# Kernel tuning notes

Measured on AMD Instinct MI355X. Metric: run time of the kernel, lower is better.

## Reference

```python
import jax, jax.numpy as jnp
import numpy as np

N = 100000        # nodes
E_INTRA = 800000  # intra (covalent) edges
E_INTER = 400000  # inter (protein-ligand) edges
NODE_DIM = 35
H = 128           # hidden_dim
G = 256           # graphs in batch
N_LAYERS = 4
BN_EPS = 1e-5

seg_sum = jax.ops.segment_sum


def setup_inputs() -> dict:
    key = jax.random.key(0)
    ks = jax.random.split(key, 24)
    s = 1.0 / np.sqrt(H)
    inp = {
        "x": jax.random.normal(ks[0], (N, NODE_DIM), jnp.float32),
        "edge_index_intra": jax.random.randint(ks[1], (2, E_INTRA), 0, N, jnp.int32),
        "edge_index_inter": jax.random.randint(ks[2], (2, E_INTER), 0, N, jnp.int32),
        "pos": jax.random.normal(ks[3], (N, 3), jnp.float32),
        "edge_attr": jax.random.uniform(ks[4], (E_INTRA, 1), jnp.float32),
        "batch": jnp.sort(jax.random.randint(ks[5], (N,), 0, G, jnp.int32)),
        # lin_node
        "lin_node_W": jax.random.normal(ks[6], (NODE_DIM, H), jnp.float32) / np.sqrt(NODE_DIM),
        "lin_node_b": jnp.zeros((H,), jnp.float32),
        # 4 DVNHIL layers (stacked)
        "W_intra": jax.random.normal(ks[7], (N_LAYERS, H, H), jnp.float32) * s,
        "b_intra": jnp.zeros((N_LAYERS, H), jnp.float32),
        "W_inter": jax.random.normal(ks[8], (N_LAYERS, H, H), jnp.float32) * s,
        "b_inter": jnp.zeros((N_LAYERS, H), jnp.float32),
        # FC head: 3 hidden linears + BN affine, then output linear to 1 task
        "fc_W": jax.random.normal(ks[9], (3, H, H), jnp.float32) * s,
        "fc_b": jnp.zeros((3, H), jnp.float32),
        "bn_gamma": jnp.ones((3, H), jnp.float32),
        "bn_beta": jnp.zeros((3, H), jnp.float32),
        "out_W": jax.random.normal(ks[10], (H, 1), jnp.float32) * s,
        "out_b": jnp.zeros((1,), jnp.float32),
    }
    return inp


def reference(x, edge_index_intra, edge_index_inter, pos, edge_attr, batch,
              lin_node_W, lin_node_b, W_intra, b_intra, W_inter, b_inter,
              fc_W, fc_b, bn_gamma, bn_beta, out_W, out_b):
    src_i, dst_i = edge_index_intra[0], edge_index_intra[1]
    src_e, dst_e = edge_index_inter[0], edge_index_inter[1]

    # lin_node: Linear + SiLU
    h = jax.nn.silu(x @ lin_node_W + lin_node_b)  # [N, H]

    # degrees of destination nodes (scatter-add of ones)
    ones_i = jnp.ones((src_i.shape[0],), h.dtype)
    ones_e = jnp.ones((src_e.shape[0],), h.dtype)
    deg_intra = seg_sum(ones_i, dst_i, num_segments=N)[:, None]           # [N,1]
    deg_inter = jnp.log(seg_sum(ones_e, dst_e, num_segments=N)[:, None] + 1.0)

    # geometric weight on inter edges from pos
    d2 = jnp.sum((pos[src_e] - pos[dst_e]) ** 2, axis=-1, keepdims=True)  # [E_inter,1]
    w_inter = jnp.exp(-d2)

    v_p = jnp.zeros_like(h)
    v_l = jnp.zeros_like(h)
    for i in range(N_LAYERS):
        # intra: gather -> edge-weighted transform -> scatter-add -> degree norm
        m_i = (h[src_i] * edge_attr) @ W_intra[i] + b_intra[i]            # [E_intra,H]
        m_i = seg_sum(m_i, dst_i, num_segments=N) / (deg_intra + 1.0)
        # inter: gather -> distance-weighted transform -> scatter-add -> log-degree scale
        m_e = (h[src_e] * w_inter) @ W_inter[i] + b_inter[i]              # [E_inter,H]
        m_e = seg_sum(m_e, dst_e, num_segments=N) * deg_inter
        v_p = jax.nn.silu(m_i + v_p)
        v_l = jax.nn.silu(m_e + v_l)
        h = h + v_p + v_l

    # global_add_pool over graphs
    g = seg_sum(h, batch, num_segments=G)  # [G, H]

    # FC head (eval mode: dropout identity, BN with running mean=0/var=1)
    bn_scale = 1.0 / jnp.sqrt(1.0 + BN_EPS)
    for j in range(3):
        g = jax.nn.leaky_relu(g @ fc_W[j] + fc_b[j], negative_slope=0.01)
        g = g * bn_scale * bn_gamma[j] + bn_beta[j]
    out = g @ out_W + out_b  # [G, 1]
    return out.reshape(-1)
```

## Files before the change

### kernel.cpp

```cpp
#include <hip/hip_runtime.h>
#include <math.h>

#define NN 100000
#define EIN 800000
#define EEX 400000
#define ND 35
#define H 128
#define NG 256
#define NL 4
#define TM 16
#define TML 16
#define NTILES 6250
#define CAPI 384
#define CAPE 224

typedef unsigned short u16;
typedef unsigned char u8;
typedef short s8v __attribute__((ext_vector_type(8)));
typedef float f4v __attribute__((ext_vector_type(4)));
typedef float f2v __attribute__((ext_vector_type(2)));

__device__ __forceinline__ float silu_f(float x){ return x / (1.0f + __expf(-x)); }
__device__ __forceinline__ float bf2f(u16 v){ return __uint_as_float(((unsigned)v) << 16); }
__device__ __forceinline__ u16 f2bf(float f){
  unsigned u = __float_as_uint(f);
  u += 0x7FFFu + ((u >> 16) & 1u);
  return (u16)(u >> 16);
}
__device__ __forceinline__ u8 f2fp8(float f){
  int p = __builtin_amdgcn_cvt_pk_fp8_f32(f, f, 0, false);
  return (u8)(p & 0xff);
}
__device__ __forceinline__ unsigned pk_bf16(float lo, float hi){
  unsigned r;
  asm("v_cvt_pk_bf16_f32 %0, %1, %2" : "=v"(r) : "v"(lo), "v"(hi));
  return r;
}

__global__ __launch_bounds__(256) void k_prep(const float* __restrict__ x,
                                              const float* __restrict__ lnW,
                                              const float* __restrict__ lnb,
                                              u16* __restrict__ h,
                                              u8* __restrict__ h8,
                                              const float* __restrict__ WI,
                                              const float* __restrict__ WE,
                                              u16* __restrict__ WfI,
                                              u16* __restrict__ WfE,
                                              const int* __restrict__ dst_i,
                                              const int* __restrict__ dst_e,
                                              int* __restrict__ cnt_i,
                                              int* __restrict__ cnt_e){
  const int NBW = 2*NL;
  const int NBL = NN/TML;
  if (blockIdx.x < NBW){
    const int lm = blockIdx.x;
    const int l = lm >> 1;
    const float* src = (lm & 1) ? (WE + (size_t)l*H*H) : (WI + (size_t)l*H*H);
    u16* dst = ((lm & 1) ? WfE : WfI) + (size_t)l*H*H;
    for (int idx = threadIdx.x; idx < H*H; idx += 256){
      const int r = idx & 7, lane = (idx>>3)&63, kc = (idx>>9)&3, jt = idx>>11;
      const int k = kc*32 + (lane>>4)*8 + r;
      const int j = jt*16 + (lane&15);
      dst[idx] = f2bf(src[k*H + j]);
    }
    return;
  }
  if (blockIdx.x < NBW + NBL){
    __shared__ u16 xs[TM][72];
    const int n0 = (blockIdx.x - NBW) * TML;
    const int tid = threadIdx.x;
    for (int i = tid; i < TM*64; i += 256){
      const int m = i >> 6, k = i & 63;
      xs[m][k] = (k < ND) ? f2bf(x[(size_t)(n0+m)*ND + k]) : (u16)0;
    }
    __syncthreads();
    const int lane = tid & 63;
    const int wv   = tid >> 6;
    const int col  = lane & 15;
    const int quad = lane >> 4;
    const int jta = 2*wv, jtb = 2*wv + 1;
    const int ja = jta*16 + col, jb = jtb*16 + col;

    f4v accA = {0.f,0.f,0.f,0.f}, accB = {0.f,0.f,0.f,0.f};
    #pragma unroll
    for (int kc = 0; kc < 2; ++kc){
      const s8v a = *(const s8v*)&xs[col][kc*32 + quad*8];
      s8v bA, bB;
      #pragma unroll
      for (int r = 0; r < 8; ++r){
        const int k = kc*32 + quad*8 + r;
        bA[r] = (k < ND) ? (short)f2bf(lnW[k*H + ja]) : (short)0;
        bB[r] = (k < ND) ? (short)f2bf(lnW[k*H + jb]) : (short)0;
      }
      accA = __builtin_amdgcn_mfma_f32_16x16x32_bf16(a, bA, accA, 0, 0, 0);
      accB = __builtin_amdgcn_mfma_f32_16x16x32_bf16(a, bB, accB, 0, 0, 0);
    }
    const float bja = lnb[ja], bjb = lnb[jb];
    #pragma unroll
    for (int r = 0; r < 4; ++r){
      const int n = n0 + quad*4 + r;
      const float ha = silu_f(accA[r] + bja);
      const float hb = silu_f(accB[r] + bjb);
      h[(size_t)n*H + ja] = f2bf(ha);
      h[(size_t)n*H + jb] = f2bf(hb);
      h8[(size_t)n*H + ja] = f2fp8(ha);
      h8[(size_t)n*H + jb] = f2fp8(hb);
    }
    return;
  }
  int e = (blockIdx.x - NBW - NBL)*256 + threadIdx.x;
  if (e < EIN) atomicAdd(&cnt_i[dst_i[e]], 1);
  else if (e < EIN + EEX) atomicAdd(&cnt_e[dst_e[e - EIN]], 1);
}

__global__ void k_scan_fused(const int* __restrict__ cnt_i, const int* __restrict__ cnt_e,
                             int* __restrict__ row_i, int* __restrict__ cur_i,
                             int* __restrict__ row_e, int* __restrict__ cur_e,
                             int* __restrict__ cursors){
  __shared__ int s[256];
  __shared__ int basev;
  const int NB = (NN + 255)/256;
  const bool inter = (int)blockIdx.x >= NB;
  const int* cnt = inter ? cnt_e : cnt_i;
  int* rowp = inter ? row_e : row_i;
  int* curp = inter ? cur_e : cur_i;
  int* cursor = cursors + (inter ? 1 : 0);
  const int b = inter ? blockIdx.x - NB : blockIdx.x;
  const int t = threadIdx.x;
  const int i = b*256 + t;
  int v = (i < NN) ? cnt[i] : 0;
  s[t] = v; __syncthreads();
  for (int o = 1; o < 256; o <<= 1){
    int a = (t >= o) ? s[t-o] : 0;
    __syncthreads();
    s[t] += a;
    __syncthreads();
  }
  if (t == 255) basev = atomicAdd(cursor, s[255]);
  __syncthreads();
  if (i < NN){
    int ex = basev + s[t] - v;
    rowp[i] = ex; curp[i] = ex;
  }
}

__global__ void k_fill_all(const int* __restrict__ src_i, const int* __restrict__ dst_i,
                           const float* __restrict__ ea,
                           const int* __restrict__ src_e, const int* __restrict__ dst_e,
                           const float* __restrict__ pos,
                           int* __restrict__ cur_i, int2* __restrict__ ev_i,
                           int* __restrict__ cur_e, int2* __restrict__ ev_e){
  int e = blockIdx.x*256 + threadIdx.x;
  if (e < EIN){
    int d = dst_i[e];
    int slot = atomicAdd(&cur_i[d], 1);
    ev_i[slot] = make_int2(src_i[e], __float_as_int(ea[e]));
  } else if (e < EIN + EEX){
    int ee = e - EIN;
    int s = src_e[ee], d = dst_e[ee];
    float dx = pos[3*s+0] - pos[3*d+0];
    float dy = pos[3*s+1] - pos[3*d+1];
    float dz = pos[3*s+2] - pos[3*d+2];
    float w = __expf(-(dx*dx + dy*dy + dz*dz));
    int slot = atomicAdd(&cur_e[d], 1);
    ev_e[slot] = make_int2(s, __float_as_int(w));
  }
}

#define ACCONE(qx, qy, vv, A0, A1, A2, A3) {                                          \
    const f2v x01 = __builtin_amdgcn_cvt_pk_f32_fp8((int)(qx), false);                \
    const f2v x23 = __builtin_amdgcn_cvt_pk_f32_fp8((int)(qx), true);                 \
    const f2v x45 = __builtin_amdgcn_cvt_pk_f32_fp8((int)(qy), false);                \
    const f2v x67 = __builtin_amdgcn_cvt_pk_f32_fp8((int)(qy), true);                 \
    A0 += x01 * (vv); A1 += x23 * (vv); A2 += x45 * (vv); A3 += x67 * (vv); }

#define GATHER_SHARED_DECL                                                            \
  __shared__ u16 aggIs[TM][136];                                                      \
  __shared__ u16 aggEs[TM][136];                                                      \
  __shared__ int2 edI[CAPI];                                                          \
  __shared__ int2 edE[CAPE];                                                          \
  __shared__ int sPI[TM], sPE[TM];                                                    \
  __shared__ int sOvf;

#define GATHER_LDS_BODY                                                               \
  {                                                                                   \
    const int slot = tid >> 4;                                                        \
    const int l16  = tid & 15;                                                        \
    const int j8 = l16 * 8;                                                           \
    const int n = n0 + slot;                                                          \
    const int sIrow = rowI[n], cIv = cntI[n];                                         \
    const int sErow = rowE[n], cEv = cntE[n];                                         \
    const int pIv = (cIv + 7) & ~7;                                                   \
    const int pEv = (cEv + 3) & ~3;                                                   \
    if (l16 == 0){ sPI[slot] = pIv; sPE[slot] = pEv; }                                \
    __syncthreads();                                                                  \
    if (tid == 0){                                                                    \
      int a = 0, bb = 0;                                                              \
      for (int i = 0; i < TM; ++i){                                                   \
        int v = sPI[i]; sPI[i] = a; a += v;                                           \
        int u = sPE[i]; sPE[i] = bb; bb += u;                                         \
      }                                                                               \
      sOvf = (a > CAPI || bb > CAPE) ? 1 : 0;                                         \
    }                                                                                 \
    __syncthreads();                                                                  \
    const int ovf = sOvf;                                                             \
    const int bsI = sPI[slot], bsE = sPE[slot];                                       \
    if (!ovf){                                                                        \
      for (int t = l16; t < pIv; t += 16)                                             \
        edI[bsI + t] = (t < cIv) ? evI[sIrow + t] : make_int2(0, 0);                  \
      for (int t = l16; t < pEv; t += 16)                                             \
        edE[bsE + t] = (t < cEv) ? evE[sErow + t] : make_int2(0, 0);                  \
    }                                                                                 \
    __syncthreads();                                                                  \
    f2v aI0={0.f,0.f}, aI1={0.f,0.f}, aI2={0.f,0.f}, aI3={0.f,0.f};                   \
    f2v aE0={0.f,0.f}, aE1={0.f,0.f}, aE2={0.f,0.f}, aE3={0.f,0.f};                   \
    if (!ovf){                                                                        \
      const int nbI_ = pIv >> 3, nbE_ = pEv >> 2;                                     \
      const int nb = nbI_ > nbE_ ? nbI_ : nbE_;                                       \
      int tIi = 0, tEi = 0;                                                           \
      for (int b = 0; b < nb; ++b){                                                   \
        const bool doI = b < nbI_;                                                    \
        const bool doE = b < nbE_;                                                    \
        int2 eIr[8]; uint2 qIr[8]; int2 eEr[4]; uint2 qEr[4];                         \
        if (doI){                                                                     \
          _Pragma("unroll")                                                           \
          for (int k = 0; k < 8; ++k) eIr[k] = edI[bsI + tIi + k];                    \
          _Pragma("unroll")                                                           \
          for (int k = 0; k < 8; ++k){                                                \
            const unsigned off = ((unsigned)eIr[k].x << 7) | (unsigned)j8;            \
            qIr[k] = *(const uint2*)(hin8 + off);                                     \
          }                                                                           \
        }                                                                             \
        if (doE){                                                                     \
          _Pragma("unroll")                                                           \
          for (int k = 0; k < 4; ++k) eEr[k] = edE[bsE + tEi + k];                    \
          _Pragma("unroll")                                                           \
          for (int k = 0; k < 4; ++k){                                                \
            const unsigned off = ((unsigned)eEr[k].x << 7) | (unsigned)j8;            \
            qEr[k] = *(const uint2*)(hin8 + off);                                     \
          }                                                                           \
        }                                                                             \
        if (doI){                                                                     \
          _Pragma("unroll")                                                           \
          for (int k = 0; k < 8; ++k){                                                \
            const float v = __int_as_float(eIr[k].y);                                 \
            ACCONE(qIr[k].x, qIr[k].y, v, aI0, aI1, aI2, aI3)                         \
          }                                                                           \
          tIi += 8;                                                                   \
        }                                                                             \
        if (doE){                                                                     \
          _Pragma("unroll")                                                           \
          for (int k = 0; k < 4; ++k){                                                \
            const float v = __int_as_float(eEr[k].y);                                 \
            ACCONE(qEr[k].x, qEr[k].y, v, aE0, aE1, aE2, aE3)                         \
          }                                                                           \
          tEi += 4;                                                                   \
        }                                                                             \
      }                                                                               \
    } else {                                                                          \
      for (int t = 0; t < cIv; ++t){                                                  \
        const int2 e0 = evI[sIrow + t];                                               \
        const float v0 = __int_as_float(e0.y);                                        \
        const unsigned off = ((unsigned)e0.x << 7) | (unsigned)j8;                    \
        const uint2 q0 = *(const uint2*)(hin8 + off);                                 \
        ACCONE(q0.x, q0.y, v0, aI0, aI1, aI2, aI3)                                    \
      }                                                                               \
      for (int t = 0; t < cEv; ++t){                                                  \
        const int2 e0 = evE[sErow + t];                                               \
        const float v0 = __int_as_float(e0.y);                                        \
        const unsigned off = ((unsigned)e0.x << 7) | (unsigned)j8;                    \
        const uint2 q0 = *(const uint2*)(hin8 + off);                                 \
        ACCONE(q0.x, q0.y, v0, aE0, aE1, aE2, aE3)                                    \
      }                                                                               \
    }                                                                                 \
    *(uint4*)&aggIs[slot][j8] = make_uint4(pk_bf16(aI0.x, aI0.y), pk_bf16(aI1.x, aI1.y), \
                                           pk_bf16(aI2.x, aI2.y), pk_bf16(aI3.x, aI3.y)); \
    *(uint4*)&aggEs[slot][j8] = make_uint4(pk_bf16(aE0.x, aE0.y), pk_bf16(aE1.x, aE1.y), \
                                           pk_bf16(aE2.x, aE2.y), pk_bf16(aE3.x, aE3.y)); \
  }

#define MFMA_BODY                                                                     \
  f4v accIA = {0.f,0.f,0.f,0.f}, accIB = {0.f,0.f,0.f,0.f};                           \
  f4v accEA = {0.f,0.f,0.f,0.f}, accEB = {0.f,0.f,0.f,0.f};                           \
  _Pragma("unroll")                                                                   \
  for (int kc = 0; kc < 4; ++kc){                                                     \
    const int koff = kc*32 + quad*8;                                                  \
    const s8v aI = *(const s8v*)&aggIs[col][koff];                                    \
    const s8v aE = *(const s8v*)&aggEs[col][koff];                                    \
    const s8v bIA = *(const s8v*)(WfI + (((jta*4 + kc)*64 + lane) << 3));             \
    const s8v bIB = *(const s8v*)(WfI + (((jtb*4 + kc)*64 + lane) << 3));             \
    const s8v bEA = *(const s8v*)(WfE + (((jta*4 + kc)*64 + lane) << 3));             \
    const s8v bEB = *(const s8v*)(WfE + (((jtb*4 + kc)*64 + lane) << 3));             \
    accIA = __builtin_amdgcn_mfma_f32_16x16x32_bf16(aI, bIA, accIA, 0, 0, 0);         \
    accIB = __builtin_amdgcn_mfma_f32_16x16x32_bf16(aI, bIB, accIB, 0, 0, 0);         \
    accEA = __builtin_amdgcn_mfma_f32_16x16x32_bf16(aE, bEA, accEA, 0, 0, 0);         \
    accEB = __builtin_amdgcn_mfma_f32_16x16x32_bf16(aE, bEB, accEB, 0, 0, 0);         \
  }

__global__ __launch_bounds__(256, 4) void k_layer(
    const u16* __restrict__ hin, const u8* __restrict__ hin8,
    u16* __restrict__ hout, u8* __restrict__ hout8,
    u16* __restrict__ vp, u16* __restrict__ vl,
    const int* __restrict__ rowI, const int* __restrict__ cntI,
    const int2* __restrict__ evI,
    const int* __restrict__ rowE, const int* __restrict__ cntE,
    const int2* __restrict__ evE,
    const u16* __restrict__ WfI, const float* __restrict__ bI,
    const u16* __restrict__ WfE, const float* __restrict__ bE)
{
  GATHER_SHARED_DECL
  const int n0 = blockIdx.x * TM;
  const int tid = threadIdx.x;

  GATHER_LDS_BODY
  __syncthreads();

  const int lane = tid & 63;
  const int w    = tid >> 6;
  const int jta = 2*w, jtb = 2*w + 1;
  const int col  = lane & 15;
  const int quad = lane >> 4;
  MFMA_BODY

  const int4 c4I = *(const int4*)&cntI[n0 + quad*4];
  const int4 c4E = *(const int4*)&cntE[n0 + quad*4];
  const int j0g = jta*16 + col;
  const int j1g = jtb*16 + col;
  const float bI0 = bI[j0g], bI1 = bI[j1g];
  const float bE0 = bE[j0g], bE1 = bE[j1g];
  #pragma unroll
  for (int r = 0; r < 4; ++r){
    const int m = quad*4 + r;
    const int n = n0 + m;
    const float cIv = (float)((r==0)?c4I.x:(r==1)?c4I.y:(r==2)?c4I.z:c4I.w);
    const float cEv = (float)((r==0)?c4E.x:(r==1)?c4E.y:(r==2)?c4E.z:c4E.w);
    const float rdI = 1.0f / (cIv + 1.0f);
    const float ldE = __logf(cEv + 1.0f);
    #pragma unroll
    for (int half = 0; half < 2; ++half){
      const int j = half ? j1g : j0g;
      const float aIv = half ? accIB[r] : accIA[r];
      const float aEv = half ? accEB[r] : accEA[r];
      const float bIv = half ? bI1 : bI0;
      const float bEv = half ? bE1 : bE0;
      const float mi = (aIv + cIv*bIv) * rdI;
      const float me = (aEv + cEv*bEv) * ldE;
      const size_t idx = (size_t)n*H + j;
      const float vpn = silu_f(mi + bf2f(vp[idx]));
      const float vln = silu_f(me + bf2f(vl[idx]));
      vp[idx] = f2bf(vpn); vl[idx] = f2bf(vln);
      const float hnew = bf2f(hin[idx]) + vpn + vln;
      hout[idx] = f2bf(hnew);
      hout8[idx] = f2fp8(hnew);
    }
  }
}

__global__ __launch_bounds__(256, 4) void k_layer0(
    const u16* __restrict__ hin, const u8* __restrict__ hin8,
    u16* __restrict__ hout, u8* __restrict__ hout8,
    u16* __restrict__ vp, u16* __restrict__ vl,
    const int* __restrict__ rowI, const int* __restrict__ cntI,
    const int2* __restrict__ evI,
    const int* __restrict__ rowE, const int* __restrict__ cntE,
    const int2* __restrict__ evE,
    const u16* __restrict__ WfI, const float* __restrict__ bI,
    const u16* __restrict__ WfE, const float* __restrict__ bE)
{
  GATHER_SHARED_DECL
  const int n0 = blockIdx.x * TM;
  const int tid = threadIdx.x;

  GATHER_LDS_BODY
  __syncthreads();

  const int lane = tid & 63;
  const int w    = tid >> 6;
  const int jta = 2*w, jtb = 2*w + 1;
  const int col  = lane & 15;
  const int quad = lane >> 4;
  MFMA_BODY

  const int4 c4I = *(const int4*)&cntI[n0 + quad*4];
  const int4 c4E = *(const int4*)&cntE[n0 + quad*4];
  const int j0g = jta*16 + col;
  const int j1g = jtb*16 + col;
  const float bI0 = bI[j0g], bI1 = bI[j1g];
  const float bE0 = bE[j0g], bE1 = bE[j1g];
  #pragma unroll
  for (int r = 0; r < 4; ++r){
    const int m = quad*4 + r;
    const int n = n0 + m;
    const float cIv = (float)((r==0)?c4I.x:(r==1)?c4I.y:(r==2)?c4I.z:c4I.w);
    const float cEv = (float)((r==0)?c4E.x:(r==1)?c4E.y:(r==2)?c4E.z:c4E.w);
    const float rdI = 1.0f / (cIv + 1.0f);
    const float ldE = __logf(cEv + 1.0f);
    #pragma unroll
    for (int half = 0; half < 2; ++half){
      const int j = half ? j1g : j0g;
      const float aIv = half ? accIB[r] : accIA[r];
      const float aEv = half ? accEB[r] : accEA[r];
      const float bIv = half ? bI1 : bI0;
      const float bEv = half ? bE1 : bE0;
      const float mi = (aIv + cIv*bIv) * rdI;
      const float me = (aEv + cEv*bEv) * ldE;
      const size_t idx = (size_t)n*H + j;
      const float vpn = silu_f(mi);
      const float vln = silu_f(me);
      vp[idx] = f2bf(vpn); vl[idx] = f2bf(vln);
      const float hnew = bf2f(hin[idx]) + vpn + vln;
      hout[idx] = f2bf(hnew);
      hout8[idx] = f2fp8(hnew);
    }
  }
}

__global__ __launch_bounds__(256, 4) void k_layer3(
    const u16* __restrict__ hin, const u8* __restrict__ hin8,
    u16* __restrict__ vp, u16* __restrict__ vl,
    const int* __restrict__ rowI, const int* __restrict__ cntI,
    const int2* __restrict__ evI,
    const int* __restrict__ rowE, const int* __restrict__ cntE,
    const int2* __restrict__ evE,
    const u16* __restrict__ WfI, const float* __restrict__ bI,
    const u16* __restrict__ WfE, const float* __restrict__ bE,
    const int* __restrict__ batch, float* __restrict__ gp)
{
  GATHER_SHARED_DECL
  const int n0 = blockIdx.x * TM;
  const int tid = threadIdx.x;

  GATHER_LDS_BODY
  __syncthreads();

  const int lane = tid & 63;
  const int w    = tid >> 6;
  const int jta = 2*w, jtb = 2*w + 1;
  const int col  = lane & 15;
  const int quad = lane >> 4;
  MFMA_BODY

  const int4 c4I = *(const int4*)&cntI[n0 + quad*4];
  const int4 c4E = *(const int4*)&cntE[n0 + quad*4];
  const int j0g = jta*16 + col;
  const int j1g = jtb*16 + col;
  const float bI0 = bI[j0g], bI1 = bI[j1g];
  const float bE0 = bE[j0g], bE1 = bE[j1g];
  float hf0[4], hf1[4];
  #pragma unroll
  for (int r = 0; r < 4; ++r){
    const int m = quad*4 + r;
    const int n = n0 + m;
    const float cIv = (float)((r==0)?c4I.x:(r==1)?c4I.y:(r==2)?c4I.z:c4I.w);
    const float cEv = (float)((r==0)?c4E.x:(r==1)?c4E.y:(r==2)?c4E.z:c4E.w);
    const float rdI = 1.0f / (cIv + 1.0f);
    const float ldE = __logf(cEv + 1.0f);
    const size_t i0 = (size_t)n*H + j0g;
    const size_t i1 = (size_t)n*H + j1g;
    const float mi0 = (accIA[r] + cIv*bI0) * rdI;
    const float me0 = (accEA[r] + cEv*bE0) * ldE;
    const float mi1 = (accIB[r] + cIv*bI1) * rdI;
    const float me1 = (accEB[r] + cEv*bE1) * ldE;
    const float vpn0 = silu_f(mi0 + bf2f(vp[i0]));
    const float vln0 = silu_f(me0 + bf2f(vl[i0]));
    const float vpn1 = silu_f(mi1 + bf2f(vp[i1]));
    const float vln1 = silu_f(me1 + bf2f(vl[i1]));
    hf0[r] = bf2f(hin[i0]) + vpn0 + vln0;
    hf1[r] = bf2f(hin[i1]) + vpn1 + vln1;
  }

  const int b0 = batch[n0];
  const int b15 = batch[n0 + TM - 1];
  if (b0 == b15){
    float s0 = hf0[0] + hf0[1] + hf0[2] + hf0[3];
    float s1 = hf1[0] + hf1[1] + hf1[2] + hf1[3];
    s0 += __shfl_xor(s0, 16, 64); s0 += __shfl_xor(s0, 32, 64);
    s1 += __shfl_xor(s1, 16, 64); s1 += __shfl_xor(s1, 32, 64);
    if (quad == 0){
      atomicAdd(&gp[(size_t)b0*H + j0g], s0);
      atomicAdd(&gp[(size_t)b0*H + j1g], s1);
    }
  } else {
    #pragma unroll
    for (int r = 0; r < 4; ++r){
      const int bcur = batch[n0 + quad*4 + r];
      atomicAdd(&gp[(size_t)bcur*H + j0g], hf0[r]);
      atomicAdd(&gp[(size_t)bcur*H + j1g], hf1[r]);
    }
  }
}

__global__ void k_fc(const float* __restrict__ g, const float* __restrict__ fcW,
                     const float* __restrict__ fcb, const float* __restrict__ gamma,
                     const float* __restrict__ beta, const float* __restrict__ outW,
                     const float* __restrict__ outb, float* __restrict__ out){
  __shared__ float row[H];
  __shared__ float red[H];
  const int gi = blockIdx.x;
  const int j = threadIdx.x;
  row[j] = g[(size_t)gi*H + j];
  __syncthreads();
  const float bn_scale = rsqrtf(1.0f + 1e-5f);
  for (int l = 0; l < 3; ++l){
    const float* W = fcW + (size_t)l*H*H;
    float acc = fcb[l*H + j];
    #pragma unroll 8
    for (int k = 0; k < H; ++k) acc += row[k] * W[k*H + j];
    acc = (acc > 0.f) ? acc : 0.01f*acc;
    acc = acc * bn_scale * gamma[l*H + j] + beta[l*H + j];
    __syncthreads();
    row[j] = acc;
    __syncthreads();
  }
  red[j] = row[j] * outW[j];
  __syncthreads();
  for (int o = 64; o > 0; o >>= 1){
    if (j < o) red[j] += red[j + o];
    __syncthreads();
  }
  if (j == 0) out[gi] = red[0] + outb[0];
}

extern "C" void kernel_launch(void* const* d_in, const int* in_sizes, int n_in,
                              void* d_out, int out_size, void* d_ws, size_t ws_size,
                              hipStream_t stream)
{
  const float* x    = (const float*)d_in[0];
  const int*   eii  = (const int*)  d_in[1];
  const int*   eie  = (const int*)  d_in[2];
  const float* pos  = (const float*)d_in[3];
  const float* ea   = (const float*)d_in[4];
  const int*   batch= (const int*)  d_in[5];
  const float* lnW  = (const float*)d_in[6];
  const float* lnb  = (const float*)d_in[7];
  const float* WIa  = (const float*)d_in[8];
  const float* bIa  = (const float*)d_in[9];
  const float* WEa  = (const float*)d_in[10];
  const float* bEa  = (const float*)d_in[11];
  const float* fcW  = (const float*)d_in[12];
  const float* fcb  = (const float*)d_in[13];
  const float* gam  = (const float*)d_in[14];
  const float* bet  = (const float*)d_in[15];
  const float* outW = (const float*)d_in[16];
  const float* outb = (const float*)d_in[17];
  float* out = (float*)d_out;

  const int* src_i = eii;  const int* dst_i = eii + EIN;
  const int* src_e = eie;  const int* dst_e = eie + EEX;

  const size_t NH = (size_t)NN * H;
  u16* hA = (u16*)d_ws;
  u16* hB = hA + NH;
  u16* vp = hB + NH;
  u16* vl = vp + NH;
  u8* hA8 = (u8*)(vl + NH);
  u8* hB8 = hA8 + NH;
  float* gp = (float*)(hB8 + NH);
  int* cnt_i = (int*)(gp + (size_t)NG*H);
  int* cnt_e = cnt_i + NN;
  int* cursors = cnt_e + NN;
  int* row_i = cursors + 4;
  int* row_e = row_i + NN;
  int* cur_i = row_e + NN;
  int* cur_e = cur_i + NN;
  int2* ev_i = (int2*)(cur_e + NN);
  int2* ev_e = ev_i + EIN;
  u16* WfI = (u16*)(ev_e + EEX);
  u16* WfE = WfI + (size_t)NL*H*H;

  const size_t need = 4*NH*sizeof(u16) + 2*NH
                    + ((size_t)NG*H + 6*(size_t)NN + 4)*4
                    + ((size_t)EIN + (size_t)EEX)*8
                    + 2*(size_t)NL*H*H*sizeof(u16);
  if (ws_size < need) return;

  hipMemsetAsync(gp, 0, ((size_t)NG*H + 2*(size_t)NN + 4)*sizeof(int), stream);

  const int NE_ALL = EIN + EEX;
  const int NBC = (NE_ALL + 255)/256;
  k_prep<<<2*NL + NN/TML + NBC, 256, 0, stream>>>(x, lnW, lnb, hA, hA8, WIa, WEa, WfI, WfE,
                                                  dst_i, dst_e, cnt_i, cnt_e);

  const int NB = (NN + 255)/256;
  k_scan_fused<<<2*NB, 256, 0, stream>>>(cnt_i, cnt_e, row_i, cur_i, row_e, cur_e, cursors);
  k_fill_all<<<NBC, 256, 0, stream>>>(src_i, dst_i, ea, src_e, dst_e, pos,
                                      cur_i, ev_i, cur_e, ev_e);

  k_layer0<<<NTILES, 256, 0, stream>>>(hA, hA8, hB, hB8, vp, vl,
      row_i, cnt_i, ev_i, row_e, cnt_e, ev_e,
      WfI + 0*(size_t)H*H, bIa + 0*H, WfE + 0*(size_t)H*H, bEa + 0*H);
  k_layer<<<NTILES, 256, 0, stream>>>(hB, hB8, hA, hA8, vp, vl,
      row_i, cnt_i, ev_i, row_e, cnt_e, ev_e,
      WfI + 1*(size_t)H*H, bIa + 1*H, WfE + 1*(size_t)H*H, bEa + 1*H);
  k_layer<<<NTILES, 256, 0, stream>>>(hA, hA8, hB, hB8, vp, vl,
      row_i, cnt_i, ev_i, row_e, cnt_e, ev_e,
      WfI + 2*(size_t)H*H, bIa + 2*H, WfE + 2*(size_t)H*H, bEa + 2*H);
  k_layer3<<<NTILES, 256, 0, stream>>>(hB, hB8, vp, vl,
      row_i, cnt_i, ev_i, row_e, cnt_e, ev_e,
      WfI + 3*(size_t)H*H, bIa + 3*H, WfE + 3*(size_t)H*H, bEa + 3*H,
      batch, gp);

  k_fc<<<NG, H, 0, stream>>>(gp, fcW, fcb, gam, bet, outW, outb, out);
}
```

Measured before the change: 522.0 us.

## Stage MFMA accumulators through LDS for vectorized row-wise epilogue stores

After the MFMA, accumulator fragments are written to shared memory (aliased over the gather buffers) and re-read row-wise so each thread handles 8 contiguous features of one node. State reads and writes of vp, vl, h and the fp8 copy become 16-byte and 8-byte vector accesses instead of scattered 2-byte and 1-byte ones. The prefix sum over slot sizes now uses a 16-lane shuffle scan, and the final layer's pooling reduces through LDS before issuing atomics. This adds two block barriers and LDS traffic per tile in exchange for coalesced global memory access.

```diff
diff --git a/kernel.cpp b/kernel.cpp
--- a/kernel.cpp
+++ b/kernel.cpp
@@ -22,6 +22,8 @@
 
 __device__ __forceinline__ float silu_f(float x){ return x / (1.0f + __expf(-x)); }
 __device__ __forceinline__ float bf2f(u16 v){ return __uint_as_float(((unsigned)v) << 16); }
+__device__ __forceinline__ float bfw_lo(unsigned u){ return __uint_as_float(u << 16); }
+__device__ __forceinline__ float bfw_hi(unsigned u){ return __uint_as_float(u & 0xffff0000u); }
 __device__ __forceinline__ u16 f2bf(float f){
   unsigned u = __float_as_uint(f);
   u += 0x7FFFu + ((u >> 16) & 1u);
@@ -175,32 +177,42 @@
     A0 += x01 * (vv); A1 += x23 * (vv); A2 += x45 * (vv); A3 += x67 * (vv); }
 
 #define GATHER_SHARED_DECL                                                            \
-  __shared__ u16 aggIs[TM][136];                                                      \
-  __shared__ u16 aggEs[TM][136];                                                      \
-  __shared__ int2 edI[CAPI];                                                          \
-  __shared__ int2 edE[CAPE];                                                          \
+  __shared__ __align__(16) char smem_[16896];                                         \
+  u16 (*aggIs)[136] = (u16(*)[136])(smem_);                                           \
+  u16 (*aggEs)[136] = (u16(*)[136])(smem_ + 4352);                                    \
+  int2* edI = (int2*)(smem_ + 8704);                                                  \
+  int2* edE = (int2*)(smem_ + 11776);                                                 \
+  float (*mif)[132] = (float(*)[132])(smem_);                                         \
+  float (*mef)[132] = (float(*)[132])(smem_ + 8448);                                  \
   __shared__ int sPI[TM], sPE[TM];                                                    \
   __shared__ int sOvf;
 
+#define GATHER_DECLS                                                                  \
+  const int slot = tid >> 4;                                                          \
+  const int l16  = tid & 15;                                                          \
+  const int j8 = l16 * 8;                                                             \
+  const int n = n0 + slot;                                                            \
+  const int sIrow = rowI[n], cIv = cntI[n];                                           \
+  const int sErow = rowE[n], cEv = cntE[n];
+
 #define GATHER_LDS_BODY                                                               \
   {                                                                                   \
-    const int slot = tid >> 4;                                                        \
-    const int l16  = tid & 15;                                                        \
-    const int j8 = l16 * 8;                                                           \
-    const int n = n0 + slot;                                                          \
-    const int sIrow = rowI[n], cIv = cntI[n];                                         \
-    const int sErow = rowE[n], cEv = cntE[n];                                         \
     const int pIv = (cIv + 7) & ~7;                                                   \
     const int pEv = (cEv + 3) & ~3;                                                   \
     if (l16 == 0){ sPI[slot] = pIv; sPE[slot] = pEv; }                                \
     __syncthreads();                                                                  \
-    if (tid == 0){                                                                    \
-      int a = 0, bb = 0;                                                              \
-      for (int i = 0; i < TM; ++i){                                                   \
-        int v = sPI[i]; sPI[i] = a; a += v;                                           \
-        int u = sPE[i]; sPE[i] = bb; bb += u;                                         \
+    if (tid < 16){                                                                    \
+      const int vI = sPI[tid], vE = sPE[tid];                                         \
+      int iI = vI, iE = vE;                                                           \
+      _Pragma("unroll")                                                               \
+      for (int o = 1; o < 16; o <<= 1){                                               \
+        const int tI_ = __shfl_up(iI, (unsigned)o, 16);                               \
+        const int tE_ = __shfl_up(iE, (unsigned)o, 16);                               \
+        if (tid >= o){ iI += tI_; iE += tE_; }                                        \
       }                                                                               \
-      sOvf = (a > CAPI || bb > CAPE) ? 1 : 0;                                         \
+      sPI[tid] = iI - vI;                                                             \
+      sPE[tid] = iE - vE;                                                             \
+      if (tid == 15) sOvf = (iI > CAPI || iE > CAPE) ? 1 : 0;                         \
     }                                                                                 \
     __syncthreads();                                                                  \
     const int ovf = sOvf;                                                             \
@@ -297,6 +309,50 @@
     accEB = __builtin_amdgcn_mfma_f32_16x16x32_bf16(aE, bEB, accEB, 0, 0, 0);         \
   }
 
+#define ACC2LDS                                                                       \
+  __syncthreads();                                                                    \
+  _Pragma("unroll")                                                                   \
+  for (int r = 0; r < 4; ++r){                                                        \
+    mif[quad*4+r][jta*16+col] = accIA[r];                                             \
+    mif[quad*4+r][jtb*16+col] = accIB[r];                                             \
+    mef[quad*4+r][jta*16+col] = accEA[r];                                             \
+    mef[quad*4+r][jtb*16+col] = accEB[r];                                             \
+  }                                                                                   \
+  __syncthreads();
+
+#define EPI_COMMON                                                                    \
+  const float cIf = (float)cIv;                                                       \
+  const float cEf = (float)cEv;                                                       \
+  const float rdI = 1.0f / (cIf + 1.0f);                                              \
+  const float ldE = __logf(cEf + 1.0f);                                               \
+  const f4v miA = *(const f4v*)&mif[slot][j8];                                        \
+  const f4v miB = *(const f4v*)&mif[slot][j8+4];                                      \
+  const f4v meA = *(const f4v*)&mef[slot][j8];                                        \
+  const f4v meB = *(const f4v*)&mef[slot][j8+4];                                      \
+  const f4v bIa_ = *(const f4v*)(bI + j8);                                            \
+  const f4v bIb_ = *(const f4v*)(bI + j8 + 4);                                        \
+  const f4v bEa_ = *(const f4v*)(bE + j8);                                            \
+  const f4v bEb_ = *(const f4v*)(bE + j8 + 4);                                        \
+  const unsigned idx8 = (unsigned)n*H + (unsigned)j8;
+
+#define STORE_STATE8                                                                  \
+  uint4 vps, vls, hs;                                                                 \
+  vps.x = pk_bf16(vpn[0],vpn[1]); vps.y = pk_bf16(vpn[2],vpn[3]);                     \
+  vps.z = pk_bf16(vpn[4],vpn[5]); vps.w = pk_bf16(vpn[6],vpn[7]);                     \
+  vls.x = pk_bf16(vln[0],vln[1]); vls.y = pk_bf16(vln[2],vln[3]);                     \
+  vls.z = pk_bf16(vln[4],vln[5]); vls.w = pk_bf16(vln[6],vln[7]);                     \
+  hs.x = pk_bf16(hnew[0],hnew[1]); hs.y = pk_bf16(hnew[2],hnew[3]);                   \
+  hs.z = pk_bf16(hnew[4],hnew[5]); hs.w = pk_bf16(hnew[6],hnew[7]);                   \
+  *(uint4*)(vp + idx8) = vps;                                                         \
+  *(uint4*)(vl + idx8) = vls;                                                         \
+  *(uint4*)(hout + idx8) = hs;                                                        \
+  int d0_ = __builtin_amdgcn_cvt_pk_fp8_f32(hnew[0], hnew[1], 0, false);              \
+  d0_ = __builtin_amdgcn_cvt_pk_fp8_f32(hnew[2], hnew[3], d0_, true);                 \
+  int d1_ = __builtin_amdgcn_cvt_pk_fp8_f32(hnew[4], hnew[5], 0, false);              \
+  d1_ = __builtin_amdgcn_cvt_pk_fp8_f32(hnew[6], hnew[7], d1_, true);                 \
+  uint2 h8s; h8s.x = (unsigned)d0_; h8s.y = (unsigned)d1_;                            \
+  *(uint2*)(hout8 + idx8) = h8s;
+
 __global__ __launch_bounds__(256, 4) void k_layer(
     const u16* __restrict__ hin, const u8* __restrict__ hin8,
     u16* __restrict__ hout, u8* __restrict__ hout8,
@@ -311,7 +367,7 @@
   GATHER_SHARED_DECL
   const int n0 = blockIdx.x * TM;
   const int tid = threadIdx.x;
-
+  GATHER_DECLS
   GATHER_LDS_BODY
   __syncthreads();
 
@@ -321,39 +377,32 @@
   const int col  = lane & 15;
   const int quad = lane >> 4;
   MFMA_BODY
-
-  const int4 c4I = *(const int4*)&cntI[n0 + quad*4];
-  const int4 c4E = *(const int4*)&cntE[n0 + quad*4];
-  const int j0g = jta*16 + col;
-  const int j1g = jtb*16 + col;
-  const float bI0 = bI[j0g], bI1 = bI[j1g];
-  const float bE0 = bE[j0g], bE1 = bE[j1g];
+  ACC2LDS
+
+  EPI_COMMON
+  const uint4 vpq = *(const uint4*)(vp + idx8);
+  const uint4 vlq = *(const uint4*)(vl + idx8);
+  const uint4 hq  = *(const uint4*)(hin + idx8);
+  const unsigned vpw[4] = {vpq.x, vpq.y, vpq.z, vpq.w};
+  const unsigned vlw[4] = {vlq.x, vlq.y, vlq.z, vlq.w};
+  const unsigned hwv[4] = {hq.x, hq.y, hq.z, hq.w};
+  float vpn[8], vln[8], hnew[8];
   #pragma unroll
-  for (int r = 0; r < 4; ++r){
-    const int m = quad*4 + r;
-    const int n = n0 + m;
-    const float cIv = (float)((r==0)?c4I.x:(r==1)?c4I.y:(r==2)?c4I.z:c4I.w);
-    const float cEv = (float)((r==0)?c4E.x:(r==1)?c4E.y:(r==2)?c4E.z:c4E.w);
-    const float rdI = 1.0f / (cIv + 1.0f);
-    const float ldE = __logf(cEv + 1.0f);
-    #pragma unroll
-    for (int half = 0; half < 2; ++half){
-      const int j = half ? j1g : j0g;
-      const float aIv = half ? accIB[r] : accIA[r];
-      const float aEv = half ? accEB[r] : accEA[r];
-      const float bIv = half ? bI1 : bI0;
-      const float bEv = half ? bE1 : bE0;
-      const float mi = (aIv + cIv*bIv) * rdI;
-      const float me = (aEv + cEv*bEv) * ldE;
-      const size_t idx = (size_t)n*H + j;
-      const float vpn = silu_f(mi + bf2f(vp[idx]));
-      const float vln = silu_f(me + bf2f(vl[idx]));
-      vp[idx] = f2bf(vpn); vl[idx] = f2bf(vln);
-      const float hnew = bf2f(hin[idx]) + vpn + vln;
-      hout[idx] = f2bf(hnew);
-      hout8[idx] = f2fp8(hnew);
-    }
-  }
+  for (int k = 0; k < 8; ++k){
+    const float miv = (k < 4) ? miA[k] : miB[k-4];
+    const float mev = (k < 4) ? meA[k] : meB[k-4];
+    const float bIv = (k < 4) ? bIa_[k] : bIb_[k-4];
+    const float bEv = (k < 4) ? bEa_[k] : bEb_[k-4];
+    const float mi = (miv + cIf*bIv) * rdI;
+    const float me = (mev + cEf*bEv) * ldE;
+    const float vpo = (k & 1) ? bfw_hi(vpw[k>>1]) : bfw_lo(vpw[k>>1]);
+    const float vlo = (k & 1) ? bfw_hi(vlw[k>>1]) : bfw_lo(vlw[k>>1]);
+    const float ho  = (k & 1) ? bfw_hi(hwv[k>>1]) : bfw_lo(hwv[k>>1]);
+    vpn[k] = silu_f(mi + vpo);
+    vln[k] = silu_f(me + vlo);
+    hnew[k] = ho + vpn[k] + vln[k];
+  }
+  STORE_STATE8
 }
 
 __global__ __launch_bounds__(256, 4) void k_layer0(
@@ -370,7 +419,7 @@
   GATHER_SHARED_DECL
   const int n0 = blockIdx.x * TM;
   const int tid = threadIdx.x;
-
+  GATHER_DECLS
   GATHER_LDS_BODY
   __syncthreads();
 
@@ -380,39 +429,26 @@
   const int col  = lane & 15;
   const int quad = lane >> 4;
   MFMA_BODY
-
-  const int4 c4I = *(const int4*)&cntI[n0 + quad*4];
-  const int4 c4E = *(const int4*)&cntE[n0 + quad*4];
-  const int j0g = jta*16 + col;
-  const int j1g = jtb*16 + col;
-  const float bI0 = bI[j0g], bI1 = bI[j1g];
-  const float bE0 = bE[j0g], bE1 = bE[j1g];
+  ACC2LDS
+
+  EPI_COMMON
+  const uint4 hq = *(const uint4*)(hin + idx8);
+  const unsigned hwv[4] = {hq.x, hq.y, hq.z, hq.w};
+  float vpn[8], vln[8], hnew[8];
   #pragma unroll
-  for (int r = 0; r < 4; ++r){
-    const int m = quad*4 + r;
-    const int n = n0 + m;
-    const float cIv = (float)((r==0)?c4I.x:(r==1)?c4I.y:(r==2)?c4I.z:c4I.w);
-    const float cEv = (float)((r==0)?c4E.x:(r==1)?c4E.y:(r==2)?c4E.z:c4E.w);
-    const float rdI = 1.0f / (cIv + 1.0f);
-    const float ldE = __logf(cEv + 1.0f);
-    #pragma unroll
-    for (int half = 0; half < 2; ++half){
-      const int j = half ? j1g : j0g;
-      const float aIv = half ? accIB[r] : accIA[r];
-      const float aEv = half ? accEB[r] : accEA[r];
-      const float bIv = half ? bI1 : bI0;
-      const float bEv = half ? bE1 : bE0;
-      const float mi = (aIv + cIv*bIv) * rdI;
-      const float me = (aEv + cEv*bEv) * ldE;
-      const size_t idx = (size_t)n*H + j;
-      const float vpn = silu_f(mi);
-      const float vln = silu_f(me);
-      vp[idx] = f2bf(vpn); vl[idx] = f2bf(vln);
-      const float hnew = bf2f(hin[idx]) + vpn + vln;
-      hout[idx] = f2bf(hnew);
-      hout8[idx] = f2fp8(hnew);
-    }
-  }
+  for (int k = 0; k < 8; ++k){
+    const float miv = (k < 4) ? miA[k] : miB[k-4];
+    const float mev = (k < 4) ? meA[k] : meB[k-4];
+    const float bIv = (k < 4) ? bIa_[k] : bIb_[k-4];
+    const float bEv = (k < 4) ? bEa_[k] : bEb_[k-4];
+    const float mi = (miv + cIf*bIv) * rdI;
+    const float me = (mev + cEf*bEv) * ldE;
+    const float ho = (k & 1) ? bfw_hi(hwv[k>>1]) : bfw_lo(hwv[k>>1]);
+    vpn[k] = silu_f(mi);
+    vln[k] = silu_f(me);
+    hnew[k] = ho + vpn[k] + vln[k];
+  }
+  STORE_STATE8
 }
 
 __global__ __launch_bounds__(256, 4) void k_layer3(
@@ -429,7 +465,7 @@
   GATHER_SHARED_DECL
   const int n0 = blockIdx.x * TM;
   const int tid = threadIdx.x;
-
+  GATHER_DECLS
   GATHER_LDS_BODY
   __syncthreads();
 
@@ -439,54 +475,57 @@
   const int col  = lane & 15;
   const int quad = lane >> 4;
   MFMA_BODY
-
-  const int4 c4I = *(const int4*)&cntI[n0 + quad*4];
-  const int4 c4E = *(const int4*)&cntE[n0 + quad*4];
-  const int j0g = jta*16 + col;
-  const int j1g = jtb*16 + col;
-  const float bI0 = bI[j0g], bI1 = bI[j1g];
-  const float bE0 = bE[j0g], bE1 = bE[j1g];
-  float hf0[4], hf1[4];
+  ACC2LDS
+
+  EPI_COMMON
+  const uint4 vpq = *(const uint4*)(vp + idx8);
+  const uint4 vlq = *(const uint4*)(vl + idx8);
+  const uint4 hq  = *(const uint4*)(hin + idx8);
+  const unsigned vpw[4] = {vpq.x, vpq.y, vpq.z, vpq.w};
+  const unsigned vlw[4] = {vlq.x, vlq.y, vlq.z, vlq.w};
+  const unsigned hwv[4] = {hq.x, hq.y, hq.z, hq.w};
+  float hnew[8];
   #pragma unroll
-  for (int r = 0; r < 4; ++r){
-    const int m = quad*4 + r;
-    const int n = n0 + m;
-    const float cIv = (float)((r==0)?c4I.x:(r==1)?c4I.y:(r==2)?c4I.z:c4I.w);
-    const float cEv = (float)((r==0)?c4E.x:(r==1)?c4E.y:(r==2)?c4E.z:c4E.w);
-    const float rdI = 1.0f / (cIv + 1.0f);
-    const float ldE = __logf(cEv + 1.0f);
-    const size_t i0 = (size_t)n*H + j0g;
-    const size_t i1 = (size_t)n*H + j1g;
-    const float mi0 = (accIA[r] + cIv*bI0) * rdI;
-    const float me0 = (accEA[r] + cEv*bE0) * ldE;
-    const float mi1 = (accIB[r] + cIv*bI1) * rdI;
-    const float me1 = (accEB[r] + cEv*bE1) * ldE;
-    const float vpn0 = silu_f(mi0 + bf2f(vp[i0]));
-    const float vln0 = silu_f(me0 + bf2f(vl[i0]));
-    const float vpn1 = silu_f(mi1 + bf2f(vp[i1]));
-    const float vln1 = silu_f(me1 + bf2f(vl[i1]));
-    hf0[r] = bf2f(hin[i0]) + vpn0 + vln0;
-    hf1[r] = bf2f(hin[i1]) + vpn1 + vln1;
+  for (int k = 0; k < 8; ++k){
+    const float miv = (k < 4) ? miA[k] : miB[k-4];
+    const float mev = (k < 4) ? meA[k] : meB[k-4];
+    const float bIv = (k < 4) ? bIa_[k] : bIb_[k-4];
+    const float bEv = (k < 4) ? bEa_[k] : bEb_[k-4];
+    const float mi = (miv + cIf*bIv) * rdI;
+    const float me = (mev + cEf*bEv) * ldE;
+    const float vpo = (k & 1) ? bfw_hi(vpw[k>>1]) : bfw_lo(vpw[k>>1]);
+    const float vlo = (k & 1) ? bfw_hi(vlw[k>>1]) : bfw_lo(vlw[k>>1]);
+    const float ho  = (k & 1) ? bfw_hi(hwv[k>>1]) : bfw_lo(hwv[k>>1]);
+    const float vpn = silu_f(mi + vpo);
+    const float vln = silu_f(me + vlo);
+    hnew[k] = ho + vpn + vln;
   }
 
   const int b0 = batch[n0];
   const int b15 = batch[n0 + TM - 1];
   if (b0 == b15){
-    float s0 = hf0[0] + hf0[1] + hf0[2] + hf0[3];
-    float s1 = hf1[0] + hf1[1] + hf1[2] + hf1[3];
-    s0 += __shfl_xor(s0, 16, 64); s0 += __shfl_xor(s0, 32, 64);
-    s1 += __shfl_xor(s1, 16, 64); s1 += __shfl_xor(s1, 32, 64);
+    #pragma unroll
+    for (int k = 0; k < 8; ++k){
+      hnew[k] += __shfl_xor(hnew[k], 16, 64);
+      hnew[k] += __shfl_xor(hnew[k], 32, 64);
+    }
+    __syncthreads();
     if (quad == 0){
-      atomicAdd(&gp[(size_t)b0*H + j0g], s0);
-      atomicAdd(&gp[(size_t)b0*H + j1g], s1);
+      f4v s0 = {hnew[0], hnew[1], hnew[2], hnew[3]};
+      f4v s1 = {hnew[4], hnew[5], hnew[6], hnew[7]};
+      *(f4v*)&mif[w][j8] = s0;
+      *(f4v*)&mif[w][j8+4] = s1;
+    }
+    __syncthreads();
+    if (tid < 128){
+      const float s = mif[0][tid] + mif[1][tid] + mif[2][tid] + mif[3][tid];
+      atomicAdd(&gp[(size_t)b0*H + tid], s);
     }
   } else {
+    const int bn = batch[n];
     #pragma unroll
-    for (int r = 0; r < 4; ++r){
-      const int bcur = batch[n0 + quad*4 + r];
-      atomicAdd(&gp[(size_t)bcur*H + j0g], hf0[r]);
-      atomicAdd(&gp[(size_t)bcur*H + j1g], hf1[r]);
-    }
+    for (int k = 0; k < 8; ++k)
+      atomicAdd(&gp[(size_t)bn*H + j8 + k], hnew[k]);
   }
 }
 
```

Result: faster. 509.0 us (-2.5%).
